# Performance work log

Hardware: AMD Instinct MI355X
Metric: run time of the kernel (lower is better)

The kernel has to match this reference:

```python
import jax, jax.numpy as jnp
import numpy as np

PI = np.pi
X_MAT = jnp.array([[0.0, 1.0], [1.0, 0.0]], dtype=jnp.complex64)


def rx_mat(t):
    c = jnp.cos(t / 2) + 0j
    s = jnp.sin(t / 2) + 0j
    return jnp.stack([jnp.stack([c, -1j * s]), jnp.stack([-1j * s, c])])


def rz_mat(t):
    e = jnp.exp(-0.5j * t)
    z = jnp.zeros_like(e)
    return jnp.stack([jnp.stack([e, z]), jnp.stack([z, jnp.conj(e)])])


def apply_1q(state, U, w):
    # state: (2,)*n complex tensor; apply 2x2 U on axis w
    st = jnp.moveaxis(state, w, 0)
    st = jnp.tensordot(U, st, axes=([1], [0]))
    return jnp.moveaxis(st, 0, w)


def apply_ctrl(state, U, c, t):
    # controlled-U: apply U on target axis t when control axis c == 1
    st = jnp.moveaxis(state, (c, t), (0, 1))
    s1 = jnp.tensordot(U, st[1], axes=([1], [0]))
    st = jnp.stack([st[0], s1], axis=0)
    return jnp.moveaxis(st, (0, 1), (c, t))


def cnot(state, c, t):
    return apply_ctrl(state, X_MAT, c, t)


def init_qkv(state, rot, crx, offset):
    # ZXZ layer
    for i in range(4):
        w, idx = offset + i, 3 * i
        state = apply_1q(state, rz_mat(rot[idx]), w)
        state = apply_1q(state, rx_mat(rot[idx + 1]), w)
        state = apply_1q(state, rz_mat(rot[idx + 2]), w)
    # CRX ring
    for i, (c, t) in enumerate([(0, 1), (1, 2), (2, 3), (3, 0)]):
        state = apply_ctrl(state, rx_mat(crx[i]), offset + c, offset + t)
    # CNOT pattern
    for c, t in [(0, 1), (1, 2), (2, 3), (3, 0), (0, 3), (1, 0), (2, 1), (3, 2)]:
        state = cnot(state, offset + c, offset + t)
    # second ZXZ layer
    for i in range(4):
        w, idx = offset + i, 12 + 3 * i
        state = apply_1q(state, rz_mat(rot[idx]), w)
        state = apply_1q(state, rx_mat(rot[idx + 1]), w)
        state = apply_1q(state, rz_mat(rot[idx + 2]), w)
    return state


def exp_z(state, w):
    p = jnp.moveaxis(jnp.abs(state) ** 2, w, 0)
    return jnp.sum(p[0]) - jnp.sum(p[1])


def exp_x(state, w):
    return jnp.real(jnp.sum(jnp.conj(state) * jnp.flip(state, axis=w)))


def score_circuit(xq, xk, wq_rot, wq_crx, wk_rot, wk_crx):
    state = jnp.zeros((2,) * 8, jnp.complex64).at[(0,) * 8].set(1.0)
    for w in range(4):  # AngleEmbedding (RX) of xq on wires 0-3
        state = apply_1q(state, rx_mat(xq[w]), w)
    state = init_qkv(state, wq_rot, wq_crx, 0)
    for w in range(4):  # AngleEmbedding (RX) of xk on wires 0-3
        state = apply_1q(state, rx_mat(xk[w]), w)
    state = init_qkv(state, wk_rot, wk_crx, 4)
    for c, t in [(0, 4), (4, 0), (1, 5), (5, 1), (2, 6), (6, 2), (3, 7), (7, 3)]:
        state = cnot(state, c, t)
    zs = [exp_z(state, w) for w in (1, 2, 3, 4)]
    xs = [exp_x(state, w) for w in (1, 2, 3, 4)]
    return jnp.stack(zs + xs)


def value_circuit(xv, score4, wv_rot, wv_crx):
    state = jnp.zeros((2,) * 4, jnp.complex64).at[(0,) * 4].set(1.0)
    for w in range(4):  # AngleEmbedding (RX) of xv
        state = apply_1q(state, rx_mat(xv[w]), w)
    state = init_qkv(state, wv_rot, wv_crx, 0)
    for w in range(4):
        state = apply_1q(state, rx_mat(jnp.tanh(score4[w]) * PI), w)
    for c, t in [(0, 1), (1, 2), (2, 3), (3, 0)]:
        state = cnot(state, c, t)
    zs = [exp_z(state, w) for w in range(4)]
    xs = [exp_x(state, w) for w in range(4)]
    return jnp.stack(zs + xs)


def setup_inputs():
    key = jax.random.key(0)
    ks = jax.random.split(key, 10)
    B, IN, D = 8192, 96, 4
    u = lambda k: jax.random.uniform(k, (24,), jnp.float32, -PI / 2, PI / 2)
    g = lambda k: 0.1 * jax.random.normal(k, (8,), jnp.float32)
    return {
        "x1": jax.random.normal(ks[0], (B, IN), jnp.float32),
        "x2": jax.random.normal(ks[1], (B, IN), jnp.float32),
        "W_pre": jax.random.normal(ks[2], (D, IN), jnp.float32) / np.sqrt(IN),
        "b_pre": jnp.zeros((D,), jnp.float32),
        "wq_rot": u(ks[3]), "wq_crx": g(ks[4]),
        "wk_rot": u(ks[5]), "wk_crx": g(ks[6]),
        "wv_rot": u(ks[7]), "wv_crx": g(ks[8]),
    }


def reference(x1, x2, W_pre, b_pre, wq_rot, wq_crx, wk_rot, wk_crx, wv_rot, wv_crx):
    x1p = x1 @ W_pre.T + b_pre  # [B,4] pre_net
    x2p = x2 @ W_pre.T + b_pre
    score = jax.vmap(score_circuit, in_axes=(0, 0, None, None, None, None))(
        x1p, x2p, wq_rot, wq_crx, wk_rot, wk_crx)  # [B,8] = [Z1..Z4, X1..X4]
    mag = jnp.sqrt(score[:, :4] ** 2 + score[:, 4:] ** 2)  # [B,4]
    out = jax.vmap(value_circuit, in_axes=(0, 0, None, None))(x2p, mag, wv_rot, wv_crx)
    return out.astype(jnp.float32)  # [B,8]
```

## Files before the change

### kernel.cpp

```cpp
#include <hip/hip_runtime.h>
#include <math.h>

#define PI_F 3.14159265358979323846f
typedef unsigned int uint;


template<int CTRL>
__device__ __forceinline__ float dppf(float x) {
    return __int_as_float(__builtin_amdgcn_update_dpp(
        0, __float_as_int(x), CTRL, 0xF, 0xF, true));
}

template<int W>
__device__ __forceinline__ float shx(float x) {
    if constexpr (W == 1) return dppf<0xB1>(x);
    else if constexpr (W == 2) return dppf<0x4E>(x);
    else if constexpr (W == 4) return dppf<0x1B>(dppf<0x141>(x));
    else return dppf<0x128>(x);
}

__device__ __forceinline__ float xorf(float x, uint u) {
    return __int_as_float(__float_as_int(x) ^ u);
}

__device__ __forceinline__ float red16(float v) {
    v += dppf<0xB1>(v);
    v += dppf<0x4E>(v);
    v += dppf<0x141>(v);
    v += dppf<0x128>(v);
    return v;
}

template<int W>
__device__ __forceinline__ void su2g(float &ar, float &ai, float4 g, uint sgn) {
    float Ai = xorf(g.y, sgn);
    float Br = xorf(g.z, sgn);
    float pr = shx<W>(ar), pi = shx<W>(ai);
    float nr = g.x*ar - Ai*ai + Br*pr - g.w*pi;
    float ni = g.x*ai + Ai*ar + Br*pi + g.w*pr;
    ar = nr; ai = ni;
}

template<int W>
__device__ __forceinline__ void rxg(float &ar, float &ai, float c, float s) {
    float pr = shx<W>(ar), pi = shx<W>(ai);
    float nr = fmaf(s, pi, c*ar);
    float ni = fmaf(-s, pr, c*ai);
    ar = nr; ai = ni;
}

template<int C, int W>
__device__ __forceinline__ void crxg(float &ar, float &ai, float2 cs, int lane) {
    bool ctl = (lane & C) != 0;
    float ec = ctl ? cs.x : 1.0f;
    float es = ctl ? cs.y : 0.0f;
    float pr = shx<W>(ar), pi = shx<W>(ai);
    float nr = fmaf(es, pi, ec*ar);
    float ni = fmaf(-es, pr, ec*ai);
    ar = nr; ai = ni;
}

template<int C, int W>
__device__ __forceinline__ void cnotg(float &ar, float &ai, int lane) {
    float pr = shx<W>(ar), pi = shx<W>(ai);
    bool ctl = (lane & C) != 0;
    ar = ctl ? pr : ar;
    ai = ctl ? pi : ai;
}

__device__ __forceinline__ void init16(float &ar, float &ai,
        const float4* su, const float2* cx, int lane,
        uint s8, uint s4, uint s2, uint s1) {
    su2g<8>(ar, ai, su[0], s8);
    su2g<4>(ar, ai, su[1], s4);
    su2g<2>(ar, ai, su[2], s2);
    su2g<1>(ar, ai, su[3], s1);
    crxg<8,4>(ar, ai, cx[0], lane);
    crxg<4,2>(ar, ai, cx[1], lane);
    crxg<2,1>(ar, ai, cx[2], lane);
    crxg<1,8>(ar, ai, cx[3], lane);
    cnotg<8,4>(ar, ai, lane);
    cnotg<4,2>(ar, ai, lane);
    cnotg<2,1>(ar, ai, lane);
    cnotg<1,8>(ar, ai, lane);
    cnotg<8,1>(ar, ai, lane);
    cnotg<4,8>(ar, ai, lane);
    cnotg<2,4>(ar, ai, lane);
    cnotg<1,2>(ar, ai, lane);
    su2g<8>(ar, ai, su[4], s8);
    su2g<4>(ar, ai, su[5], s4);
    su2g<2>(ar, ai, su[6], s2);
    su2g<1>(ar, ai, su[7], s1);
}

__global__ __launch_bounds__(256) void qa_fused(
        const float* __restrict__ x1, const float* __restrict__ x2,
        const float* __restrict__ W, const float* __restrict__ b,
        const float* __restrict__ wq_rot, const float* __restrict__ wq_crx,
        const float* __restrict__ wk_rot, const float* __restrict__ wk_crx,
        const float* __restrict__ wv_rot, const float* __restrict__ wv_crx,
        float* __restrict__ out, int B) {
    __shared__ float4 s_su[24];
    __shared__ float2 s_cx[12];
    __shared__ float  s_kc[8];

    int t = threadIdx.x;
    if (t < 36) {
        if (t < 24) {
            int ini = t >> 3, g = t & 7;
            const float* rp = (ini == 0) ? wq_rot : (ini == 1) ? wk_rot : wv_rot;
            int base = (g & 4) ? 12 + 3*(g & 3) : 3*(g & 3);
            float t0 = rp[base], t1 = rp[base+1], t2 = rp[base+2];
            float hp = 0.5f*(t0+t2), hm = 0.5f*(t0-t2), h1 = 0.5f*t1;
            float cp = __cosf(hp), sp = __sinf(hp);
            float cm = __cosf(hm), sm = __sinf(hm);
            float c1 = __cosf(h1), s1v = __sinf(h1);
            s_su[t] = make_float4(c1*cp, -c1*sp, s1v*sm, -s1v*cm);
        } else {
            int j = t - 24;
            int ini = j >> 2, idx = j & 3;
            const float* cp = (ini == 0) ? wq_crx : (ini == 1) ? wk_crx : wv_crx;
            float a = cp[idx] * 0.5f;
            s_cx[j] = make_float2(__cosf(a), __sinf(a));
        }
    }
    __syncthreads();

    int lane = t & 15;
    uint s8 = (lane & 8) ? 0x80000000u : 0u;
    uint s4 = (lane & 4) ? 0x80000000u : 0u;
    uint s2 = (lane & 2) ? 0x80000000u : 0u;
    uint s1 = (lane & 1) ? 0x80000000u : 0u;

    if (t < 16) {
        float kr = (lane == 0) ? 1.f : 0.f, ki = 0.f;
        init16(kr, ki, s_su + 8, s_cx + 4, lane, s8, s4, s2, s1);
        float p = kr*kr + ki*ki;
        float cZ1 = red16(xorf(p, s4));
        float cZ2 = red16(xorf(p, s2));
        float cZ3 = red16(xorf(p, s1));
        float cZ4 = red16(xorf(p, s8));
        float cX1 = red16(kr*shx<4>(kr) + ki*shx<4>(ki));
        float cX2 = red16(kr*shx<2>(kr) + ki*shx<2>(ki));
        float cX3 = red16(kr*shx<1>(kr) + ki*shx<1>(ki));
        if (lane == 0) {
            s_kc[0]=cZ1; s_kc[1]=cZ2; s_kc[2]=cZ3; s_kc[3]=cZ4;
            s_kc[4]=cX1; s_kc[5]=cX2; s_kc[6]=cX3;
        }
    }
    __syncthreads();

    int e = blockIdx.x * 16 + (t >> 4);
    if (e >= B) return;

    float a10=0,a11=0,a12=0,a13=0, a20=0,a21=0,a22=0,a23=0;
    const float* x1r = x1 + (size_t)e*96 + lane;
    const float* x2r = x2 + (size_t)e*96 + lane;
#pragma unroll
    for (int j = 0; j < 6; ++j) {
        float v1 = x1r[16*j], v2 = x2r[16*j];
        float w0 = W[0*96 + 16*j + lane];
        float w1 = W[1*96 + 16*j + lane];
        float w2 = W[2*96 + 16*j + lane];
        float w3 = W[3*96 + 16*j + lane];
        a10 = fmaf(v1,w0,a10); a11 = fmaf(v1,w1,a11);
        a12 = fmaf(v1,w2,a12); a13 = fmaf(v1,w3,a13);
        a20 = fmaf(v2,w0,a20); a21 = fmaf(v2,w1,a21);
        a22 = fmaf(v2,w2,a22); a23 = fmaf(v2,w3,a23);
    }
    a10 = red16(a10); a11 = red16(a11); a12 = red16(a12); a13 = red16(a13);
    a20 = red16(a20); a21 = red16(a21); a22 = red16(a22); a23 = red16(a23);
    float bx = b[0], by = b[1], bz = b[2], bw = b[3];
    float hq0 = 0.5f*(a10+bx), hq1 = 0.5f*(a11+by), hq2 = 0.5f*(a12+bz), hq3 = 0.5f*(a13+bw);
    float hk0 = 0.5f*(a20+bx), hk1 = 0.5f*(a21+by), hk2 = 0.5f*(a22+bz), hk3 = 0.5f*(a23+bw);
    float cq0 = __cosf(hq0), sq0 = __sinf(hq0);
    float cq1 = __cosf(hq1), sq1 = __sinf(hq1);
    float cq2 = __cosf(hq2), sq2 = __sinf(hq2);
    float cq3 = __cosf(hq3), sq3 = __sinf(hq3);
    float ck0 = __cosf(hk0), sk0 = __sinf(hk0);
    float ck1 = __cosf(hk1), sk1 = __sinf(hk1);
    float ck2 = __cosf(hk2), sk2 = __sinf(hk2);
    float ck3 = __cosf(hk3), sk3 = __sinf(hk3);

    float ar = (lane == 0) ? 1.f : 0.f, ai = 0.f;
    rxg<8>(ar,ai,cq0,sq0);
    rxg<4>(ar,ai,cq1,sq1);
    rxg<2>(ar,ai,cq2,sq2);
    rxg<1>(ar,ai,cq3,sq3);
    init16(ar, ai, s_su + 0, s_cx + 0, lane, s8, s4, s2, s1);
    rxg<8>(ar,ai,ck0,sk0);
    rxg<4>(ar,ai,ck1,sk1);
    rxg<2>(ar,ai,ck2,sk2);
    rxg<1>(ar,ai,ck3,sk3);

    float p = ar*ar + ai*ai;
    float zw0 = red16(xorf(p, s8));
    float xw0 = red16(ar*shx<8>(ar) + ai*shx<8>(ai));
    float xw1 = red16(ar*shx<4>(ar) + ai*shx<4>(ai));
    float xw2 = red16(ar*shx<2>(ar) + ai*shx<2>(ai));
    float xw3 = red16(ar*shx<1>(ar) + ai*shx<1>(ai));

    float cZ1 = s_kc[0], cZ2 = s_kc[1], cZ3 = s_kc[2], cZ4 = s_kc[3];
    float cX1 = s_kc[4], cX2 = s_kc[5], cX3 = s_kc[6];
    float X1 = xw1*cX1, X2 = xw2*cX2, X3 = xw3*cX3, Z4 = zw0*cZ4;
    float mag0 = sqrtf(fmaf(cZ1,cZ1,X1*X1));
    float mag1 = sqrtf(fmaf(cZ2,cZ2,X2*X2));
    float mag2 = sqrtf(fmaf(cZ3,cZ3,X3*X3));
    float mag3 = sqrtf(fmaf(Z4,Z4,xw0*xw0));
    float e20 = __expf(2.f*mag0), e21 = __expf(2.f*mag1);
    float e22 = __expf(2.f*mag2), e23 = __expf(2.f*mag3);
    float hv0 = 0.5f*PI_F*(e20-1.f)/(e20+1.f);
    float hv1 = 0.5f*PI_F*(e21-1.f)/(e21+1.f);
    float hv2 = 0.5f*PI_F*(e22-1.f)/(e22+1.f);
    float hv3 = 0.5f*PI_F*(e23-1.f)/(e23+1.f);
    float cv0 = __cosf(hv0), sv0 = __sinf(hv0);
    float cv1 = __cosf(hv1), sv1 = __sinf(hv1);
    float cv2 = __cosf(hv2), sv2 = __sinf(hv2);
    float cv3 = __cosf(hv3), sv3 = __sinf(hv3);

    ar = (lane == 0) ? 1.f : 0.f; ai = 0.f;
    rxg<8>(ar,ai,ck0,sk0);
    rxg<4>(ar,ai,ck1,sk1);
    rxg<2>(ar,ai,ck2,sk2);
    rxg<1>(ar,ai,ck3,sk3);
    init16(ar, ai, s_su + 16, s_cx + 8, lane, s8, s4, s2, s1);
    rxg<8>(ar,ai,cv0,sv0);
    rxg<4>(ar,ai,cv1,sv1);
    rxg<2>(ar,ai,cv2,sv2);
    rxg<1>(ar,ai,cv3,sv3);
    cnotg<8,4>(ar, ai, lane);
    cnotg<4,2>(ar, ai, lane);
    cnotg<2,1>(ar, ai, lane);
    cnotg<1,8>(ar, ai, lane);

    p = ar*ar + ai*ai;
    float zo0 = red16(xorf(p, s8));
    float zo1 = red16(xorf(p, s4));
    float zo2 = red16(xorf(p, s2));
    float zo3 = red16(xorf(p, s1));
    float xo0 = red16(ar*shx<8>(ar) + ai*shx<8>(ai));
    float xo1 = red16(ar*shx<4>(ar) + ai*shx<4>(ai));
    float xo2 = red16(ar*shx<2>(ar) + ai*shx<2>(ai));
    float xo3 = red16(ar*shx<1>(ar) + ai*shx<1>(ai));

    if (lane == 0) {
        float4* o4 = (float4*)(out + (size_t)e * 8);
        o4[0] = make_float4(zo0, zo1, zo2, zo3);
        o4[1] = make_float4(xo0, xo1, xo2, xo3);
    }
}

extern "C" void kernel_launch(void* const* d_in, const int* in_sizes, int n_in,
                              void* d_out, int out_size, void* d_ws, size_t ws_size,
                              hipStream_t stream) {
    const float* x1     = (const float*)d_in[0];
    const float* x2     = (const float*)d_in[1];
    const float* W      = (const float*)d_in[2];
    const float* b      = (const float*)d_in[3];
    const float* wq_rot = (const float*)d_in[4];
    const float* wq_crx = (const float*)d_in[5];
    const float* wk_rot = (const float*)d_in[6];
    const float* wk_crx = (const float*)d_in[7];
    const float* wv_rot = (const float*)d_in[8];
    const float* wv_crx = (const float*)d_in[9];
    float* out = (float*)d_out;
    int B = in_sizes[0] / 96;

    int blocks = (B + 15) / 16;
    qa_fused<<<blocks, 256, 0, stream>>>(x1, x2, W, b,
                                         wq_rot, wq_crx, wk_rot, wk_crx,
                                         wv_rot, wv_crx, out, B);
}
```

Before: 11.15 us.

## Process two batch elements per 16-lane group and shrink blocks to one wave

Each 16-lane group now simulates two batch elements at once, interleaving their gate sequences to expose ILP across the DPP shuffle chains. Blocks shrink to 64 threads (8 elements per block). Every group now recomputes the input-independent key-circuit constants itself, which removes the second __syncthreads and the shared-memory broadcast. The cost is higher register pressure and the constant circuit being evaluated redundantly by every group.

Result: no change. 11.08 us (-0.6%).

```diff
diff --git a/kernel.cpp b/kernel.cpp
--- a/kernel.cpp
+++ b/kernel.cpp
@@ -31,44 +31,58 @@
     return v;
 }
 
-template<int W>
-__device__ __forceinline__ void su2g(float &ar, float &ai, float4 g, uint sgn) {
+template<int W, int N>
+__device__ __forceinline__ void su2g(float (&ar)[N], float (&ai)[N], float4 g, uint sgn) {
     float Ai = xorf(g.y, sgn);
     float Br = xorf(g.z, sgn);
-    float pr = shx<W>(ar), pi = shx<W>(ai);
-    float nr = g.x*ar - Ai*ai + Br*pr - g.w*pi;
-    float ni = g.x*ai + Ai*ar + Br*pi + g.w*pr;
-    ar = nr; ai = ni;
-}
-
-template<int W>
-__device__ __forceinline__ void rxg(float &ar, float &ai, float c, float s) {
-    float pr = shx<W>(ar), pi = shx<W>(ai);
-    float nr = fmaf(s, pi, c*ar);
-    float ni = fmaf(-s, pr, c*ai);
-    ar = nr; ai = ni;
-}
-
-template<int C, int W>
-__device__ __forceinline__ void crxg(float &ar, float &ai, float2 cs, int lane) {
+#pragma unroll
+    for (int el = 0; el < N; ++el) {
+        float pr = shx<W>(ar[el]), pi = shx<W>(ai[el]);
+        float nr = g.x*ar[el] - Ai*ai[el] + Br*pr - g.w*pi;
+        float ni = g.x*ai[el] + Ai*ar[el] + Br*pi + g.w*pr;
+        ar[el] = nr; ai[el] = ni;
+    }
+}
+
+template<int W, int N>
+__device__ __forceinline__ void rxg(float (&ar)[N], float (&ai)[N],
+                                    const float (&c)[N], const float (&s)[N]) {
+#pragma unroll
+    for (int el = 0; el < N; ++el) {
+        float pr = shx<W>(ar[el]), pi = shx<W>(ai[el]);
+        float nr = fmaf(s[el], pi, c[el]*ar[el]);
+        float ni = fmaf(-s[el], pr, c[el]*ai[el]);
+        ar[el] = nr; ai[el] = ni;
+    }
+}
+
+template<int C, int W, int N>
+__device__ __forceinline__ void crxg(float (&ar)[N], float (&ai)[N], float2 cs, int lane) {
     bool ctl = (lane & C) != 0;
     float ec = ctl ? cs.x : 1.0f;
     float es = ctl ? cs.y : 0.0f;
-    float pr = shx<W>(ar), pi = shx<W>(ai);
-    float nr = fmaf(es, pi, ec*ar);
-    float ni = fmaf(-es, pr, ec*ai);
-    ar = nr; ai = ni;
-}
-
-template<int C, int W>
-__device__ __forceinline__ void cnotg(float &ar, float &ai, int lane) {
-    float pr = shx<W>(ar), pi = shx<W>(ai);
+#pragma unroll
+    for (int el = 0; el < N; ++el) {
+        float pr = shx<W>(ar[el]), pi = shx<W>(ai[el]);
+        float nr = fmaf(es, pi, ec*ar[el]);
+        float ni = fmaf(-es, pr, ec*ai[el]);
+        ar[el] = nr; ai[el] = ni;
+    }
+}
+
+template<int C, int W, int N>
+__device__ __forceinline__ void cnotg(float (&ar)[N], float (&ai)[N], int lane) {
     bool ctl = (lane & C) != 0;
-    ar = ctl ? pr : ar;
-    ai = ctl ? pi : ai;
-}
-
-__device__ __forceinline__ void init16(float &ar, float &ai,
+#pragma unroll
+    for (int el = 0; el < N; ++el) {
+        float pr = shx<W>(ar[el]), pi = shx<W>(ai[el]);
+        ar[el] = ctl ? pr : ar[el];
+        ai[el] = ctl ? pi : ai[el];
+    }
+}
+
+template<int N>
+__device__ __forceinline__ void init16(float (&ar)[N], float (&ai)[N],
         const float4* su, const float2* cx, int lane,
         uint s8, uint s4, uint s2, uint s1) {
     su2g<8>(ar, ai, su[0], s8);
@@ -93,16 +107,15 @@
     su2g<1>(ar, ai, su[7], s1);
 }
 
-__global__ __launch_bounds__(256) void qa_fused(
+__global__ __launch_bounds__(64) void qa_fused(
         const float* __restrict__ x1, const float* __restrict__ x2,
-        const float* __restrict__ W, const float* __restrict__ b,
+        const float* __restrict__ Wp, const float* __restrict__ b,
         const float* __restrict__ wq_rot, const float* __restrict__ wq_crx,
         const float* __restrict__ wk_rot, const float* __restrict__ wk_crx,
         const float* __restrict__ wv_rot, const float* __restrict__ wv_crx,
         float* __restrict__ out, int B) {
     __shared__ float4 s_su[24];
     __shared__ float2 s_cx[12];
-    __shared__ float  s_kc[8];
 
     int t = threadIdx.x;
     if (t < 36) {
@@ -127,126 +140,138 @@
     __syncthreads();
 
     int lane = t & 15;
+    int grp  = t >> 4;
     uint s8 = (lane & 8) ? 0x80000000u : 0u;
     uint s4 = (lane & 4) ? 0x80000000u : 0u;
     uint s2 = (lane & 2) ? 0x80000000u : 0u;
     uint s1 = (lane & 1) ? 0x80000000u : 0u;
 
-    if (t < 16) {
-        float kr = (lane == 0) ? 1.f : 0.f, ki = 0.f;
+    int e0 = blockIdx.x * 8 + 2*grp;
+    if (e0 >= B) return;
+    int e1 = (e0 + 1 < B) ? e0 + 1 : B - 1;
+
+    float kc[7];
+    {
+        float kr[1], ki[1];
+        kr[0] = (lane == 0) ? 1.f : 0.f; ki[0] = 0.f;
         init16(kr, ki, s_su + 8, s_cx + 4, lane, s8, s4, s2, s1);
-        float p = kr*kr + ki*ki;
-        float cZ1 = red16(xorf(p, s4));
-        float cZ2 = red16(xorf(p, s2));
-        float cZ3 = red16(xorf(p, s1));
-        float cZ4 = red16(xorf(p, s8));
-        float cX1 = red16(kr*shx<4>(kr) + ki*shx<4>(ki));
-        float cX2 = red16(kr*shx<2>(kr) + ki*shx<2>(ki));
-        float cX3 = red16(kr*shx<1>(kr) + ki*shx<1>(ki));
-        if (lane == 0) {
-            s_kc[0]=cZ1; s_kc[1]=cZ2; s_kc[2]=cZ3; s_kc[3]=cZ4;
-            s_kc[4]=cX1; s_kc[5]=cX2; s_kc[6]=cX3;
-        }
-    }
-    __syncthreads();
-
-    int e = blockIdx.x * 16 + (t >> 4);
-    if (e >= B) return;
-
-    float a10=0,a11=0,a12=0,a13=0, a20=0,a21=0,a22=0,a23=0;
-    const float* x1r = x1 + (size_t)e*96 + lane;
-    const float* x2r = x2 + (size_t)e*96 + lane;
+        float p = kr[0]*kr[0] + ki[0]*ki[0];
+        kc[0] = red16(xorf(p, s4));
+        kc[1] = red16(xorf(p, s2));
+        kc[2] = red16(xorf(p, s1));
+        kc[3] = red16(xorf(p, s8));
+        kc[4] = red16(fmaf(kr[0], shx<4>(kr[0]), ki[0]*shx<4>(ki[0])));
+        kc[5] = red16(fmaf(kr[0], shx<2>(kr[0]), ki[0]*shx<2>(ki[0])));
+        kc[6] = red16(fmaf(kr[0], shx<1>(kr[0]), ki[0]*shx<1>(ki[0])));
+    }
+
+    float A1[2][4] = {{0,0,0,0},{0,0,0,0}};
+    float A2[2][4] = {{0,0,0,0},{0,0,0,0}};
+    const float* xp1[2] = { x1 + (size_t)e0*96 + lane, x1 + (size_t)e1*96 + lane };
+    const float* xp2[2] = { x2 + (size_t)e0*96 + lane, x2 + (size_t)e1*96 + lane };
 #pragma unroll
     for (int j = 0; j < 6; ++j) {
-        float v1 = x1r[16*j], v2 = x2r[16*j];
-        float w0 = W[0*96 + 16*j + lane];
-        float w1 = W[1*96 + 16*j + lane];
-        float w2 = W[2*96 + 16*j + lane];
-        float w3 = W[3*96 + 16*j + lane];
-        a10 = fmaf(v1,w0,a10); a11 = fmaf(v1,w1,a11);
-        a12 = fmaf(v1,w2,a12); a13 = fmaf(v1,w3,a13);
-        a20 = fmaf(v2,w0,a20); a21 = fmaf(v2,w1,a21);
-        a22 = fmaf(v2,w2,a22); a23 = fmaf(v2,w3,a23);
-    }
-    a10 = red16(a10); a11 = red16(a11); a12 = red16(a12); a13 = red16(a13);
-    a20 = red16(a20); a21 = red16(a21); a22 = red16(a22); a23 = red16(a23);
-    float bx = b[0], by = b[1], bz = b[2], bw = b[3];
-    float hq0 = 0.5f*(a10+bx), hq1 = 0.5f*(a11+by), hq2 = 0.5f*(a12+bz), hq3 = 0.5f*(a13+bw);
-    float hk0 = 0.5f*(a20+bx), hk1 = 0.5f*(a21+by), hk2 = 0.5f*(a22+bz), hk3 = 0.5f*(a23+bw);
-    float cq0 = __cosf(hq0), sq0 = __sinf(hq0);
-    float cq1 = __cosf(hq1), sq1 = __sinf(hq1);
-    float cq2 = __cosf(hq2), sq2 = __sinf(hq2);
-    float cq3 = __cosf(hq3), sq3 = __sinf(hq3);
-    float ck0 = __cosf(hk0), sk0 = __sinf(hk0);
-    float ck1 = __cosf(hk1), sk1 = __sinf(hk1);
-    float ck2 = __cosf(hk2), sk2 = __sinf(hk2);
-    float ck3 = __cosf(hk3), sk3 = __sinf(hk3);
-
-    float ar = (lane == 0) ? 1.f : 0.f, ai = 0.f;
-    rxg<8>(ar,ai,cq0,sq0);
-    rxg<4>(ar,ai,cq1,sq1);
-    rxg<2>(ar,ai,cq2,sq2);
-    rxg<1>(ar,ai,cq3,sq3);
+        float w[4];
+#pragma unroll
+        for (int d = 0; d < 4; ++d) w[d] = Wp[d*96 + 16*j + lane];
+#pragma unroll
+        for (int el = 0; el < 2; ++el) {
+            float v1 = xp1[el][16*j], v2 = xp2[el][16*j];
+#pragma unroll
+            for (int d = 0; d < 4; ++d) {
+                A1[el][d] = fmaf(v1, w[d], A1[el][d]);
+                A2[el][d] = fmaf(v2, w[d], A2[el][d]);
+            }
+        }
+    }
+    float Bv[4] = { b[0], b[1], b[2], b[3] };
+    float CQ[4][2], SQ[4][2], CK[4][2], SK[4][2];
+#pragma unroll
+    for (int el = 0; el < 2; ++el) {
+#pragma unroll
+        for (int d = 0; d < 4; ++d) {
+            float hq = 0.5f*(red16(A1[el][d]) + Bv[d]);
+            float hk = 0.5f*(red16(A2[el][d]) + Bv[d]);
+            CQ[d][el] = __cosf(hq); SQ[d][el] = __sinf(hq);
+            CK[d][el] = __cosf(hk); SK[d][el] = __sinf(hk);
+        }
+    }
+
+    float ar[2], ai[2];
+    ar[0] = (lane == 0) ? 1.f : 0.f; ar[1] = ar[0];
+    ai[0] = 0.f; ai[1] = 0.f;
+    rxg<8>(ar, ai, CQ[0], SQ[0]);
+    rxg<4>(ar, ai, CQ[1], SQ[1]);
+    rxg<2>(ar, ai, CQ[2], SQ[2]);
+    rxg<1>(ar, ai, CQ[3], SQ[3]);
     init16(ar, ai, s_su + 0, s_cx + 0, lane, s8, s4, s2, s1);
-    rxg<8>(ar,ai,ck0,sk0);
-    rxg<4>(ar,ai,ck1,sk1);
-    rxg<2>(ar,ai,ck2,sk2);
-    rxg<1>(ar,ai,ck3,sk3);
-
-    float p = ar*ar + ai*ai;
-    float zw0 = red16(xorf(p, s8));
-    float xw0 = red16(ar*shx<8>(ar) + ai*shx<8>(ai));
-    float xw1 = red16(ar*shx<4>(ar) + ai*shx<4>(ai));
-    float xw2 = red16(ar*shx<2>(ar) + ai*shx<2>(ai));
-    float xw3 = red16(ar*shx<1>(ar) + ai*shx<1>(ai));
-
-    float cZ1 = s_kc[0], cZ2 = s_kc[1], cZ3 = s_kc[2], cZ4 = s_kc[3];
-    float cX1 = s_kc[4], cX2 = s_kc[5], cX3 = s_kc[6];
-    float X1 = xw1*cX1, X2 = xw2*cX2, X3 = xw3*cX3, Z4 = zw0*cZ4;
-    float mag0 = sqrtf(fmaf(cZ1,cZ1,X1*X1));
-    float mag1 = sqrtf(fmaf(cZ2,cZ2,X2*X2));
-    float mag2 = sqrtf(fmaf(cZ3,cZ3,X3*X3));
-    float mag3 = sqrtf(fmaf(Z4,Z4,xw0*xw0));
-    float e20 = __expf(2.f*mag0), e21 = __expf(2.f*mag1);
-    float e22 = __expf(2.f*mag2), e23 = __expf(2.f*mag3);
-    float hv0 = 0.5f*PI_F*(e20-1.f)/(e20+1.f);
-    float hv1 = 0.5f*PI_F*(e21-1.f)/(e21+1.f);
-    float hv2 = 0.5f*PI_F*(e22-1.f)/(e22+1.f);
-    float hv3 = 0.5f*PI_F*(e23-1.f)/(e23+1.f);
-    float cv0 = __cosf(hv0), sv0 = __sinf(hv0);
-    float cv1 = __cosf(hv1), sv1 = __sinf(hv1);
-    float cv2 = __cosf(hv2), sv2 = __sinf(hv2);
-    float cv3 = __cosf(hv3), sv3 = __sinf(hv3);
-
-    ar = (lane == 0) ? 1.f : 0.f; ai = 0.f;
-    rxg<8>(ar,ai,ck0,sk0);
-    rxg<4>(ar,ai,ck1,sk1);
-    rxg<2>(ar,ai,ck2,sk2);
-    rxg<1>(ar,ai,ck3,sk3);
+    rxg<8>(ar, ai, CK[0], SK[0]);
+    rxg<4>(ar, ai, CK[1], SK[1]);
+    rxg<2>(ar, ai, CK[2], SK[2]);
+    rxg<1>(ar, ai, CK[3], SK[3]);
+
+    float CV[4][2], SV[4][2];
+#pragma unroll
+    for (int el = 0; el < 2; ++el) {
+        float p = ar[el]*ar[el] + ai[el]*ai[el];
+        float zw0 = red16(xorf(p, s8));
+        float xw0 = red16(fmaf(ar[el], shx<8>(ar[el]), ai[el]*shx<8>(ai[el])));
+        float xw1 = red16(fmaf(ar[el], shx<4>(ar[el]), ai[el]*shx<4>(ai[el])));
+        float xw2 = red16(fmaf(ar[el], shx<2>(ar[el]), ai[el]*shx<2>(ai[el])));
+        float xw3 = red16(fmaf(ar[el], shx<1>(ar[el]), ai[el]*shx<1>(ai[el])));
+        float X1 = xw1*kc[4], X2 = xw2*kc[5], X3 = xw3*kc[6], Z4 = zw0*kc[3];
+        float mg[4];
+        mg[0] = sqrtf(fmaf(kc[0], kc[0], X1*X1));
+        mg[1] = sqrtf(fmaf(kc[1], kc[1], X2*X2));
+        mg[2] = sqrtf(fmaf(kc[2], kc[2], X3*X3));
+        mg[3] = sqrtf(fmaf(Z4, Z4, xw0*xw0));
+#pragma unroll
+        for (int d = 0; d < 4; ++d) {
+            float e2 = __expf(2.f*mg[d]);
+            float hv = 0.5f*PI_F*(e2 - 1.f)/(e2 + 1.f);
+            CV[d][el] = __cosf(hv); SV[d][el] = __sinf(hv);
+        }
+    }
+
+    ar[0] = (lane == 0) ? 1.f : 0.f; ar[1] = ar[0];
+    ai[0] = 0.f; ai[1] = 0.f;
+    rxg<8>(ar, ai, CK[0], SK[0]);
+    rxg<4>(ar, ai, CK[1], SK[1]);
+    rxg<2>(ar, ai, CK[2], SK[2]);
+    rxg<1>(ar, ai, CK[3], SK[3]);
     init16(ar, ai, s_su + 16, s_cx + 8, lane, s8, s4, s2, s1);
-    rxg<8>(ar,ai,cv0,sv0);
-    rxg<4>(ar,ai,cv1,sv1);
-    rxg<2>(ar,ai,cv2,sv2);
-    rxg<1>(ar,ai,cv3,sv3);
+    rxg<8>(ar, ai, CV[0], SV[0]);
+    rxg<4>(ar, ai, CV[1], SV[1]);
+    rxg<2>(ar, ai, CV[2], SV[2]);
+    rxg<1>(ar, ai, CV[3], SV[3]);
     cnotg<8,4>(ar, ai, lane);
     cnotg<4,2>(ar, ai, lane);
     cnotg<2,1>(ar, ai, lane);
     cnotg<1,8>(ar, ai, lane);
 
-    p = ar*ar + ai*ai;
-    float zo0 = red16(xorf(p, s8));
-    float zo1 = red16(xorf(p, s4));
-    float zo2 = red16(xorf(p, s2));
-    float zo3 = red16(xorf(p, s1));
-    float xo0 = red16(ar*shx<8>(ar) + ai*shx<8>(ai));
-    float xo1 = red16(ar*shx<4>(ar) + ai*shx<4>(ai));
-    float xo2 = red16(ar*shx<2>(ar) + ai*shx<2>(ai));
-    float xo3 = red16(ar*shx<1>(ar) + ai*shx<1>(ai));
+    float ZO[4][2], XO[4][2];
+#pragma unroll
+    for (int el = 0; el < 2; ++el) {
+        float p = ar[el]*ar[el] + ai[el]*ai[el];
+        ZO[0][el] = red16(xorf(p, s8));
+        ZO[1][el] = red16(xorf(p, s4));
+        ZO[2][el] = red16(xorf(p, s2));
+        ZO[3][el] = red16(xorf(p, s1));
+        XO[0][el] = red16(fmaf(ar[el], shx<8>(ar[el]), ai[el]*shx<8>(ai[el])));
+        XO[1][el] = red16(fmaf(ar[el], shx<4>(ar[el]), ai[el]*shx<4>(ai[el])));
+        XO[2][el] = red16(fmaf(ar[el], shx<2>(ar[el]), ai[el]*shx<2>(ai[el])));
+        XO[3][el] = red16(fmaf(ar[el], shx<1>(ar[el]), ai[el]*shx<1>(ai[el])));
+    }
 
     if (lane == 0) {
-        float4* o4 = (float4*)(out + (size_t)e * 8);
-        o4[0] = make_float4(zo0, zo1, zo2, zo3);
-        o4[1] = make_float4(xo0, xo1, xo2, xo3);
+        float4* o0 = (float4*)(out + (size_t)e0 * 8);
+        o0[0] = make_float4(ZO[0][0], ZO[1][0], ZO[2][0], ZO[3][0]);
+        o0[1] = make_float4(XO[0][0], XO[1][0], XO[2][0], XO[3][0]);
+        if (e0 + 1 < B) {
+            float4* o1 = (float4*)(out + (size_t)(e0 + 1) * 8);
+            o1[0] = make_float4(ZO[0][1], ZO[1][1], ZO[2][1], ZO[3][1]);
+            o1[1] = make_float4(XO[0][1], XO[1][1], XO[2][1], XO[3][1]);
+        }
     }
 }
 
@@ -266,8 +291,8 @@
     float* out = (float*)d_out;
     int B = in_sizes[0] / 96;
 
-    int blocks = (B + 15) / 16;
-    qa_fused<<<blocks, 256, 0, stream>>>(x1, x2, W, b,
-                                         wq_rot, wq_crx, wk_rot, wk_crx,
-                                         wv_rot, wv_crx, out, B);
-}
+    int blocks = (B + 7) / 8;
+    qa_fused<<<blocks, 64, 0, stream>>>(x1, x2, W, b,
+                                        wq_rot, wq_crx, wk_rot, wk_crx,
+                                        wv_rot, wv_crx, out, B);
+}
```
